# Kernel tuning notes

Hardware: AMD Instinct MI355X
Metric: run time of the kernel (lower is better)

The kernel has to match this reference:

```python
import jax, jax.numpy as jnp
import numpy as np

B, D, K, M1, M2 = 256, 128, 32, 64, 32   # batch, n_nodes, K copies, dims[1], dims[2]
H1, H2, L = 128, 64, 32                   # pivae_dims


def setup_inputs() -> dict:
    key = jax.random.key(0)
    ks = iter(jax.random.split(key, 32))

    def rn(shape, scale):
        return jax.random.normal(next(ks), shape, dtype=jnp.float32) * scale

    x = jax.random.normal(next(ks), (B, D), dtype=jnp.float32)

    # per-node fc1 weights: [D, M1, D]; bounds force nonneg with zero diag column
    W1_pos = jnp.abs(rn((D, M1, D), 1.0 / np.sqrt(D)))
    W1_neg = jnp.abs(rn((D, M1, D), 1.0 / np.sqrt(D)))
    eye = jnp.eye(D, dtype=jnp.float32)[:, None, :]   # zero out W[j,:,j]
    W1_pos = W1_pos * (1.0 - eye)
    W1_neg = W1_neg * (1.0 - eye)
    b1_pos = rn((D, M1), 0.02)
    b1_neg = rn((D, M1), 0.02)

    # LocallyConnected stacks: weight [K, m_in, m_out]
    lc1_w = rn((K, M1, M2), 1.0 / np.sqrt(M1)); lc1_b = rn((K, M2), 0.02)
    lc2_w = rn((K, M2, 1), 1.0 / np.sqrt(M2));  lc2_b = rn((K, 1), 0.02)

    # per-sample beta Linear(k,1): weights [B, K], bias [B]
    beta_w = rn((B, K), 1.0 / np.sqrt(K)); beta_b = rn((B,), 0.02)

    # VAE params (encoder -> mu/logvar -> decoder), stored as (in,out) matrices
    enc1_w = rn((K, H1), 1.0 / np.sqrt(K));  enc1_b = jnp.zeros((H1,), jnp.float32)
    enc2_w = rn((H1, H2), 1.0 / np.sqrt(H1)); enc2_b = jnp.zeros((H2,), jnp.float32)
    mu_w = rn((H2, L), 1.0 / np.sqrt(H2));    mu_b = jnp.zeros((L,), jnp.float32)
    lv_w = rn((H2, L), 1.0 / np.sqrt(H2));    lv_b = jnp.zeros((L,), jnp.float32)
    dec1_w = rn((L, H2), 1.0 / np.sqrt(L));   dec1_b = jnp.zeros((H2,), jnp.float32)
    dec2_w = rn((H2, H1), 1.0 / np.sqrt(H2)); dec2_b = jnp.zeros((H1,), jnp.float32)
    dec3_w = rn((H1, K), 1.0 / np.sqrt(H1));  dec3_b = jnp.zeros((K,), jnp.float32)

    eps = jax.random.normal(next(ks), (B, L), dtype=jnp.float32)  # reparam noise

    return dict(x=x, W1_pos=W1_pos, W1_neg=W1_neg, b1_pos=b1_pos, b1_neg=b1_neg,
                lc1_w=lc1_w, lc1_b=lc1_b, lc2_w=lc2_w, lc2_b=lc2_b,
                beta_w=beta_w, beta_b=beta_b,
                enc1_w=enc1_w, enc1_b=enc1_b, enc2_w=enc2_w, enc2_b=enc2_b,
                mu_w=mu_w, mu_b=mu_b, lv_w=lv_w, lv_b=lv_b,
                dec1_w=dec1_w, dec1_b=dec1_b, dec2_w=dec2_w, dec2_b=dec2_b,
                dec3_w=dec3_w, dec3_b=dec3_b, eps=eps)


def reference(x, W1_pos, W1_neg, b1_pos, b1_neg, lc1_w, lc1_b, lc2_w, lc2_b,
              beta_w, beta_b, enc1_w, enc1_b, enc2_w, enc2_b, mu_w, mu_b,
              lv_w, lv_b, dec1_w, dec1_b, dec2_w, dec2_b, dec3_w, dec3_b, eps):
    b, d = x.shape
    k = lc1_w.shape[0]

    # fused per-node fc1: (pos - neg) applied to x with column j zeroed, all j at once
    W1 = W1_pos - W1_neg                      # [D, M1, D]
    b1 = b1_pos - b1_neg                      # [D, M1]
    full = jnp.einsum('bi,jhi->bjh', x, W1)   # as if no column were zeroed
    diagW = jnp.einsum('jhj->jh', W1)         # [D, M1] column-j weight of node j
    phi = full - x[:, :, None] * diagW[None] + b1[None]   # [B, D, M1]

    # expand to K copies, run sigmoid + LocallyConnected stack
    h = jnp.broadcast_to(phi[:, :, None, :], (b, d, k, phi.shape[-1]))
    h = jnp.einsum('bdkm,kmn->bdkn', jax.nn.sigmoid(h), lc1_w) + lc1_b   # [B,D,K,M2]
    h = jnp.einsum('bdkm,kmn->bdkn', jax.nn.sigmoid(h), lc2_w) + lc2_b   # [B,D,K,1]
    last_phi_x = h[..., 0]                    # [B, D, K]

    # per-sample beta projection (batched over B)
    y1 = jnp.einsum('bdk,bk->bd', last_phi_x, beta_w) + beta_b[:, None]

    # VAE on the stacked beta weights [B, K]
    e = jax.nn.relu(beta_w @ enc1_w + enc1_b)
    e = jax.nn.relu(e @ enc2_w + enc2_b)
    mu = e @ mu_w + mu_b
    logvar = e @ lv_w + lv_b
    z = mu + eps * jnp.exp(0.5 * logvar)
    dh = jax.nn.relu(z @ dec1_w + dec1_b)
    dh = jax.nn.relu(dh @ dec2_w + dec2_b)
    recon = dh @ dec3_w + dec3_b              # [B, K]

    y2 = jnp.einsum('bdk,bk->bd', last_phi_x, recon) + beta_b[:, None]
    return (y1, y2, mu, logvar)
```

## Files before the change

### kernel.cpp

```cpp
#include <hip/hip_runtime.h>
#include <stdint.h>

#define BB 256
#define DD 128
#define KK 32
#define MM1 64
#define MM2 32

typedef __attribute__((ext_vector_type(8))) short bf16x8;
typedef __attribute__((ext_vector_type(4))) float f32x4;

#define LOG2E 1.44269504088896f


__device__ __forceinline__ short f2b(float f) {
  uint32_t u = __builtin_bit_cast(uint32_t, f);
  u += 0x7FFFu + ((u >> 16) & 1u);
  return (short)(u >> 16);
}
__device__ __forceinline__ float sigm_pre(float acc, float cpre) {
  return __builtin_amdgcn_rcpf(
      1.0f + __builtin_amdgcn_exp2f(fmaf(acc, -LOG2E, cpre)));
}

__global__ __launch_bounds__(256) void combo_kernel(
    const float* __restrict__ x, const float* __restrict__ W1p,
    const float* __restrict__ W1n, const float* __restrict__ b1p,
    const float* __restrict__ b1n, const float* __restrict__ lc1w,
    const float* __restrict__ lc1b, const float* __restrict__ lc2b,
    const float* __restrict__ betaw,
    const float* __restrict__ enc1w, const float* __restrict__ enc1b,
    const float* __restrict__ enc2w, const float* __restrict__ enc2b,
    const float* __restrict__ muw,  const float* __restrict__ mub,
    const float* __restrict__ lvw,  const float* __restrict__ lvb,
    const float* __restrict__ dec1w, const float* __restrict__ dec1b,
    const float* __restrict__ dec2w, const float* __restrict__ dec2b,
    const float* __restrict__ dec3w, const float* __restrict__ dec3b,
    const float* __restrict__ eps,
    char* __restrict__ ws, float* __restrict__ mu_out,
    float* __restrict__ lv_out)
{
  const int bx = blockIdx.x;
  if (bx < 1024) {
    const int tid = bx * 256 + threadIdx.x;
    {
      float4 a = ((const float4*)W1p)[tid];
      float4 b = ((const float4*)W1n)[tid];
      short4 s;
      s.x = f2b(a.x - b.x); s.y = f2b(a.y - b.y);
      s.z = f2b(a.z - b.z); s.w = f2b(a.w - b.w);
      ((short4*)(ws + 303104))[tid] = s;
    }
    if (tid < 8192) {
      float4 v = ((const float4*)x)[tid];
      short4 s;
      s.x = f2b(v.x); s.y = f2b(v.y); s.z = f2b(v.z); s.w = f2b(v.w);
      ((short4*)(ws + 65536))[tid] = s;
    }
    if (tid < 65536) {
      int k = tid >> 11, n = (tid >> 6) & 31, m = tid & 63;
      ((short*)(ws + 131072))[tid] = f2b(lc1w[k * 2048 + m * 32 + n]);
    }
    if (tid < 8192) {
      ((float*)(ws + 32768))[tid] = betaw[(tid & 255) * 32 + (tid >> 8)];
    }
    if (tid < 1024) { ((float*)(ws + 262144))[tid] = -lc1b[tid] * LOG2E; }
    if (tid < 32) { ((float*)(ws + 266240))[tid] = 0.25f * lc2b[tid]; }
    if (tid < 8192) {
      ((float*)(ws + 270336))[tid] = -(b1p[tid] - b1n[tid]) * LOG2E;
    }
    return;
  }

  const int b = bx - 1024, t = threadIdx.x;
  float* reconT = (float*)ws;
  __shared__ float bw[KK], e1[128], e2[64], zz[32], d1s[64], d2s[128];
  if (t < KK) bw[t] = betaw[b * KK + t];
  __syncthreads();
  if (t < 128) {
    float a0 = enc1b[t], a1 = 0.f;
    #pragma unroll
    for (int k = 0; k < KK; k += 2) {
      a0 = fmaf(bw[k], enc1w[k * 128 + t], a0);
      a1 = fmaf(bw[k + 1], enc1w[(k + 1) * 128 + t], a1);
    }
    e1[t] = fmaxf(a0 + a1, 0.f);
  }
  __syncthreads();
  if (t < 64) {
    float a0 = enc2b[t], a1 = 0.f, a2 = 0.f, a3 = 0.f;
    #pragma unroll 8
    for (int h = 0; h < 128; h += 4) {
      a0 = fmaf(e1[h], enc2w[h * 64 + t], a0);
      a1 = fmaf(e1[h + 1], enc2w[(h + 1) * 64 + t], a1);
      a2 = fmaf(e1[h + 2], enc2w[(h + 2) * 64 + t], a2);
      a3 = fmaf(e1[h + 3], enc2w[(h + 3) * 64 + t], a3);
    }
    e2[t] = fmaxf((a0 + a1) + (a2 + a3), 0.f);
  }
  __syncthreads();
  if (t < 32) {
    float m0 = mub[t], m1 = 0.f, l0 = lvb[t], l1 = 0.f;
    #pragma unroll 8
    for (int h = 0; h < 64; h += 2) {
      float ea = e2[h], eb = e2[h + 1];
      m0 = fmaf(ea, muw[h * 32 + t], m0);
      m1 = fmaf(eb, muw[(h + 1) * 32 + t], m1);
      l0 = fmaf(ea, lvw[h * 32 + t], l0);
      l1 = fmaf(eb, lvw[(h + 1) * 32 + t], l1);
    }
    float m = m0 + m1, l = l0 + l1;
    mu_out[b * 32 + t] = m;
    lv_out[b * 32 + t] = l;
    zz[t] = fmaf(eps[b * 32 + t], __expf(0.5f * l), m);
  }
  __syncthreads();
  if (t < 64) {
    float a0 = dec1b[t], a1 = 0.f;
    #pragma unroll
    for (int l = 0; l < 32; l += 2) {
      a0 = fmaf(zz[l], dec1w[l * 64 + t], a0);
      a1 = fmaf(zz[l + 1], dec1w[(l + 1) * 64 + t], a1);
    }
    d1s[t] = fmaxf(a0 + a1, 0.f);
  }
  __syncthreads();
  if (t < 128) {
    float a0 = dec2b[t], a1 = 0.f, a2 = 0.f, a3 = 0.f;
    #pragma unroll 8
    for (int h = 0; h < 64; h += 4) {
      a0 = fmaf(d1s[h], dec2w[h * 128 + t], a0);
      a1 = fmaf(d1s[h + 1], dec2w[(h + 1) * 128 + t], a1);
      a2 = fmaf(d1s[h + 2], dec2w[(h + 2) * 128 + t], a2);
      a3 = fmaf(d1s[h + 3], dec2w[(h + 3) * 128 + t], a3);
    }
    d2s[t] = fmaxf((a0 + a1) + (a2 + a3), 0.f);
  }
  __syncthreads();
  if (t < 32) {
    float a0 = dec3b[t], a1 = 0.f, a2 = 0.f, a3 = 0.f;
    #pragma unroll 8
    for (int h = 0; h < 128; h += 4) {
      a0 = fmaf(d2s[h], dec3w[h * 32 + t], a0);
      a1 = fmaf(d2s[h + 1], dec3w[(h + 1) * 32 + t], a1);
      a2 = fmaf(d2s[h + 2], dec3w[(h + 2) * 32 + t], a2);
      a3 = fmaf(d2s[h + 3], dec3w[(h + 3) * 32 + t], a3);
    }
    reconT[t * BB + b] = (a0 + a1) + (a2 + a3);
  }
}

__global__ __launch_bounds__(1024) void main_kernel(
    const float* __restrict__ lc2w, const float* __restrict__ betab,
    const char* __restrict__ ws, float* __restrict__ out)
{
  const int bx = blockIdx.x;
  const int d2 = bx >> 2;
  const int bq = bx & 3;
  const int tid = threadIdx.x;
  const int wv = tid >> 6, lane = tid & 63;
  const int g = lane >> 4, l15 = lane & 15;

  const short* __restrict__ xbf   = (const short*)(ws + 65536);
  const short* __restrict__ lc1T  = (const short*)(ws + 131072);
  const float* __restrict__ lc1bs = (const float*)(ws + 262144);
  const float* __restrict__ lc2bq = (const float*)(ws + 266240);
  const float* __restrict__ b1s   = (const float*)(ws + 270336);
  const short* __restrict__ w1bf  = (const short*)(ws + 303104);
  const float* __restrict__ betaT = (const float*)(ws + 32768);
  const float* __restrict__ recT  = (const float*)(ws + 0);

  __shared__ __align__(16) short sS[2][64 * 64];
  __shared__ float yred[16][64][2];

  const int dsel = wv >> 3;
  const int d = d2 * 2 + dsel;

  {
    const int sub = wv & 7;
    const int bt = sub >> 1, mtp = (sub & 1) * 2;
    const short* xrow = xbf + (bq * 64 + bt * 16 + l15) * DD + g * 8;
    bf16x8 xa[4];
    #pragma unroll
    for (int ks = 0; ks < 4; ++ks)
      xa[ks] = *(const bf16x8*)(xrow + ks * 32);
    const short* wrow = w1bf + d * (MM1 * DD);
    #pragma unroll
    for (int mi = 0; mi < 2; ++mi) {
      const int m = (mtp + mi) * 16 + l15;
      f32x4 acc = {0.f, 0.f, 0.f, 0.f};
      #pragma unroll
      for (int ks = 0; ks < 4; ++ks) {
        bf16x8 wb = *(const bf16x8*)(wrow + m * DD + ks * 32 + g * 8);
        acc = __builtin_amdgcn_mfma_f32_16x16x32_bf16(xa[ks], wb, acc, 0, 0, 0);
      }
      const float cpre = b1s[d * MM1 + m];
      #pragma unroll
      for (int r = 0; r < 4; ++r) {
        const int bl = bt * 16 + g * 4 + r;
        sS[dsel][bl * 64 + ((m & ~7) ^ ((bl & 7) << 3)) + (m & 7)] =
            f2b(sigm_pre(acc[r], cpre));
      }
    }
  }
  __syncthreads();

  const int ksel = wv & 7;
  float y1p[4] = {0, 0, 0, 0}, y2p[4] = {0, 0, 0, 0};
  const short* sbase = sS[dsel];

  #pragma unroll
  for (int kk = 0; kk < 4; ++kk) {
    const int k = ksel * 4 + kk;
    const short* ap = lc1T + (k * 32 + l15) * 64 + g * 8;
    const bf16x8 A00 = *(const bf16x8*)(ap);
    const bf16x8 A01 = *(const bf16x8*)(ap + 32);
    const bf16x8 A10 = *(const bf16x8*)(ap + 16 * 64);
    const bf16x8 A11 = *(const bf16x8*)(ap + 16 * 64 + 32);
    const f32x4 c40 = *(const f32x4*)(lc1bs + k * 32 + g * 4);
    const f32x4 c41 = *(const f32x4*)(lc1bs + k * 32 + 16 + g * 4);
    const f32x4 w40 = *(const f32x4*)(lc2w + k * 32 + g * 4);
    const f32x4 w41 = *(const f32x4*)(lc2w + k * 32 + 16 + g * 4);
    const float lb = lc2bq[k];
    const float* bTk = betaT + k * BB + bq * 64 + l15;
    const float* rTk = recT + k * BB + bq * 64 + l15;

    #pragma unroll
    for (int rt = 0; rt < 4; ++rt) {
      const int b = rt * 16 + l15;
      const int bsw = (b & 7) << 3;
      const bf16x8 sa0 = *(const bf16x8*)&sbase[b * 64 + ((g * 8) ^ bsw)];
      const bf16x8 sa1 = *(const bf16x8*)&sbase[b * 64 + ((32 + g * 8) ^ bsw)];
      f32x4 a0 = {0.f, 0.f, 0.f, 0.f}, a1 = {0.f, 0.f, 0.f, 0.f};
      a0 = __builtin_amdgcn_mfma_f32_16x16x32_bf16(A00, sa0, a0, 0, 0, 0);
      a0 = __builtin_amdgcn_mfma_f32_16x16x32_bf16(A01, sa1, a0, 0, 0, 0);
      a1 = __builtin_amdgcn_mfma_f32_16x16x32_bf16(A10, sa0, a1, 0, 0, 0);
      a1 = __builtin_amdgcn_mfma_f32_16x16x32_bf16(A11, sa1, a1, 0, 0, 0);
      float v = lb;
      #pragma unroll
      for (int r = 0; r < 4; ++r) {
        v = fmaf(sigm_pre(a0[r], c40[r]), w40[r], v);
        v = fmaf(sigm_pre(a1[r], c41[r]), w41[r], v);
      }
      y1p[rt] = fmaf(v, bTk[rt * 16], y1p[rt]);
      y2p[rt] = fmaf(v, rTk[rt * 16], y2p[rt]);
    }
  }

  #pragma unroll
  for (int rt = 0; rt < 4; ++rt) {
    y1p[rt] += __shfl_xor(y1p[rt], 16, 64);
    y1p[rt] += __shfl_xor(y1p[rt], 32, 64);
    y2p[rt] += __shfl_xor(y2p[rt], 16, 64);
    y2p[rt] += __shfl_xor(y2p[rt], 32, 64);
  }
  if (g == 0) {
    #pragma unroll
    for (int rt = 0; rt < 4; ++rt) {
      yred[wv][rt * 16 + l15][0] = y1p[rt];
      yred[wv][rt * 16 + l15][1] = y2p[rt];
    }
  }
  __syncthreads();
  if (tid < 256) {
    const int o = tid & 1, bl = (tid >> 1) & 63, ds = tid >> 7;
    float s = 0.f;
    #pragma unroll
    for (int j = 0; j < 8; ++j) s += yred[ds * 8 + j][bl][o];
    const int gb = bq * 64 + bl;
    out[o * (BB * DD) + gb * DD + d2 * 2 + ds] = s + betab[gb];
  }
}

extern "C" void kernel_launch(void* const* d_in, const int* in_sizes, int n_in,
                              void* d_out, int out_size, void* d_ws, size_t ws_size,
                              hipStream_t stream) {
  const float* x     = (const float*)d_in[0];
  const float* W1p   = (const float*)d_in[1];
  const float* W1n   = (const float*)d_in[2];
  const float* b1p   = (const float*)d_in[3];
  const float* b1n   = (const float*)d_in[4];
  const float* lc1w  = (const float*)d_in[5];
  const float* lc1b  = (const float*)d_in[6];
  const float* lc2w  = (const float*)d_in[7];
  const float* lc2b  = (const float*)d_in[8];
  const float* betaw = (const float*)d_in[9];
  const float* betab = (const float*)d_in[10];
  const float* enc1w = (const float*)d_in[11];
  const float* enc1b = (const float*)d_in[12];
  const float* enc2w = (const float*)d_in[13];
  const float* enc2b = (const float*)d_in[14];
  const float* muw   = (const float*)d_in[15];
  const float* mub   = (const float*)d_in[16];
  const float* lvw   = (const float*)d_in[17];
  const float* lvb   = (const float*)d_in[18];
  const float* dec1w = (const float*)d_in[19];
  const float* dec1b = (const float*)d_in[20];
  const float* dec2w = (const float*)d_in[21];
  const float* dec2b = (const float*)d_in[22];
  const float* dec3w = (const float*)d_in[23];
  const float* dec3b = (const float*)d_in[24];
  const float* eps   = (const float*)d_in[25];

  float* out    = (float*)d_out;
  char*  ws     = (char*)d_ws;
  float* mu_out = out + BB * DD * 2;
  float* lv_out = mu_out + BB * 32;

  combo_kernel<<<dim3(1280), dim3(256), 0, stream>>>(
      x, W1p, W1n, b1p, b1n, lc1w, lc1b, lc2b, betaw,
      enc1w, enc1b, enc2w, enc2b, muw, mub, lvw, lvb,
      dec1w, dec1b, dec2w, dec2b, dec3w, dec3b, eps,
      ws, mu_out, lv_out);

  main_kernel<<<dim3(256), dim3(1024), 0, stream>>>(
      lc2w, betab, (const char*)ws, out);
}
```

Measured before the change: 135.6 us.

## Split main kernel to one node per block and stage per-k params in LDS

The main kernel now processes one node d per 512-thread block (512 blocks) instead of two nodes per 1024-thread block. Beta, recon, lc1 bias, lc2 weights and lc2 bias are first staged into shared memory, so the inner loop no longer reads them from global memory. This targets per-iteration global load latency and gives finer-grained blocks for scheduling across CUs. In exchange, each block repeats the staging loads and does its own reduction.

```diff
diff --git a/kernel.cpp b/kernel.cpp
--- a/kernel.cpp
+++ b/kernel.cpp
@@ -150,12 +150,12 @@
   }
 }
 
-__global__ __launch_bounds__(1024) void main_kernel(
+__global__ __launch_bounds__(512) void main_kernel(
     const float* __restrict__ lc2w, const float* __restrict__ betab,
     const char* __restrict__ ws, float* __restrict__ out)
 {
   const int bx = blockIdx.x;
-  const int d2 = bx >> 2;
+  const int d = bx >> 2;
   const int bq = bx & 3;
   const int tid = threadIdx.x;
   const int wv = tid >> 6, lane = tid & 63;
@@ -170,15 +170,25 @@
   const float* __restrict__ betaT = (const float*)(ws + 32768);
   const float* __restrict__ recT  = (const float*)(ws + 0);
 
-  __shared__ __align__(16) short sS[2][64 * 64];
-  __shared__ float yred[16][64][2];
-
-  const int dsel = wv >> 3;
-  const int d = d2 * 2 + dsel;
+  __shared__ __align__(16) short sS[64 * 64];
+  __shared__ __align__(16) float betaS[KK * 64];
+  __shared__ __align__(16) float reconS[KK * 64];
+  __shared__ __align__(16) float cS[KK * MM2];
+  __shared__ __align__(16) float wSS[KK * MM2];
+  __shared__ float lbq[KK];
+  __shared__ float yred[8][64][2];
 
   {
-    const int sub = wv & 7;
-    const int bt = sub >> 1, mtp = (sub & 1) * 2;
+    const int k = tid >> 4, j = (tid & 15) * 4;
+    *(float4*)&betaS[k * 64 + j]  = *(const float4*)&betaT[k * BB + bq * 64 + j];
+    *(float4*)&reconS[k * 64 + j] = *(const float4*)&recT[k * BB + bq * 64 + j];
+  }
+  if (tid < 256)      ((f32x4*)cS)[tid]        = ((const f32x4*)lc1bs)[tid];
+  else if (tid < 512) ((f32x4*)wSS)[tid - 256] = ((const f32x4*)lc2w)[tid - 256];
+  if (tid < KK) lbq[tid] = lc2bq[tid];
+
+  {
+    const int bt = wv >> 1, mtp = (wv & 1) * 2;
     const short* xrow = xbf + (bq * 64 + bt * 16 + l15) * DD + g * 8;
     bf16x8 xa[4];
     #pragma unroll
@@ -198,39 +208,35 @@
       #pragma unroll
       for (int r = 0; r < 4; ++r) {
         const int bl = bt * 16 + g * 4 + r;
-        sS[dsel][bl * 64 + ((m & ~7) ^ ((bl & 7) << 3)) + (m & 7)] =
+        sS[bl * 64 + ((m & ~7) ^ ((bl & 7) << 3)) + (m & 7)] =
             f2b(sigm_pre(acc[r], cpre));
       }
     }
   }
   __syncthreads();
 
-  const int ksel = wv & 7;
   float y1p[4] = {0, 0, 0, 0}, y2p[4] = {0, 0, 0, 0};
-  const short* sbase = sS[dsel];
 
   #pragma unroll
   for (int kk = 0; kk < 4; ++kk) {
-    const int k = ksel * 4 + kk;
+    const int k = wv * 4 + kk;
     const short* ap = lc1T + (k * 32 + l15) * 64 + g * 8;
     const bf16x8 A00 = *(const bf16x8*)(ap);
     const bf16x8 A01 = *(const bf16x8*)(ap + 32);
     const bf16x8 A10 = *(const bf16x8*)(ap + 16 * 64);
     const bf16x8 A11 = *(const bf16x8*)(ap + 16 * 64 + 32);
-    const f32x4 c40 = *(const f32x4*)(lc1bs + k * 32 + g * 4);
-    const f32x4 c41 = *(const f32x4*)(lc1bs + k * 32 + 16 + g * 4);
-    const f32x4 w40 = *(const f32x4*)(lc2w + k * 32 + g * 4);
-    const f32x4 w41 = *(const f32x4*)(lc2w + k * 32 + 16 + g * 4);
-    const float lb = lc2bq[k];
-    const float* bTk = betaT + k * BB + bq * 64 + l15;
-    const float* rTk = recT + k * BB + bq * 64 + l15;
+    const f32x4 c40 = *(const f32x4*)&cS[k * 32 + g * 4];
+    const f32x4 c41 = *(const f32x4*)&cS[k * 32 + 16 + g * 4];
+    const f32x4 w40 = *(const f32x4*)&wSS[k * 32 + g * 4];
+    const f32x4 w41 = *(const f32x4*)&wSS[k * 32 + 16 + g * 4];
+    const float lb = lbq[k];
 
     #pragma unroll
     for (int rt = 0; rt < 4; ++rt) {
       const int b = rt * 16 + l15;
       const int bsw = (b & 7) << 3;
-      const bf16x8 sa0 = *(const bf16x8*)&sbase[b * 64 + ((g * 8) ^ bsw)];
-      const bf16x8 sa1 = *(const bf16x8*)&sbase[b * 64 + ((32 + g * 8) ^ bsw)];
+      const bf16x8 sa0 = *(const bf16x8*)&sS[b * 64 + ((g * 8) ^ bsw)];
+      const bf16x8 sa1 = *(const bf16x8*)&sS[b * 64 + ((32 + g * 8) ^ bsw)];
       f32x4 a0 = {0.f, 0.f, 0.f, 0.f}, a1 = {0.f, 0.f, 0.f, 0.f};
       a0 = __builtin_amdgcn_mfma_f32_16x16x32_bf16(A00, sa0, a0, 0, 0, 0);
       a0 = __builtin_amdgcn_mfma_f32_16x16x32_bf16(A01, sa1, a0, 0, 0, 0);
@@ -242,8 +248,8 @@
         v = fmaf(sigm_pre(a0[r], c40[r]), w40[r], v);
         v = fmaf(sigm_pre(a1[r], c41[r]), w41[r], v);
       }
-      y1p[rt] = fmaf(v, bTk[rt * 16], y1p[rt]);
-      y2p[rt] = fmaf(v, rTk[rt * 16], y2p[rt]);
+      y1p[rt] = fmaf(v, betaS[k * 64 + rt * 16 + l15], y1p[rt]);
+      y2p[rt] = fmaf(v, reconS[k * 64 + rt * 16 + l15], y2p[rt]);
     }
   }
 
@@ -262,13 +268,13 @@
     }
   }
   __syncthreads();
-  if (tid < 256) {
-    const int o = tid & 1, bl = (tid >> 1) & 63, ds = tid >> 7;
+  if (tid < 128) {
+    const int bl = tid >> 1, o = tid & 1;
     float s = 0.f;
     #pragma unroll
-    for (int j = 0; j < 8; ++j) s += yred[ds * 8 + j][bl][o];
-    const int gb = bq * 64 + bl;
-    out[o * (BB * DD) + gb * DD + d2 * 2 + ds] = s + betab[gb];
+    for (int w = 0; w < 8; ++w) s += yred[w][bl][o];
+    const int b = bq * 64 + bl;
+    out[o * (BB * DD) + b * DD + d] = s + betab[b];
   }
 }
 
@@ -313,6 +319,6 @@
       dec1w, dec1b, dec2w, dec2b, dec3w, dec3b, eps,
       ws, mu_out, lv_out);
 
-  main_kernel<<<dim3(256), dim3(1024), 0, stream>>>(
+  main_kernel<<<dim3(512), dim3(512), 0, stream>>>(
       lc2w, betab, (const char*)ws, out);
 }
```

Measured after the change: 135.4 us. No clear change (-0.2%).
